# Optimization experiments

Hardware: AMD Instinct MI355X
Metric: run time of the kernel (lower is better)

Reference implementation:

```python
import jax, jax.numpy as jnp
import numpy as np

NUM_STEPS = 3
NUM_HEADS = 8
HEAD_DIM = 128
EPS = 1e-5


def layernorm(x, g, b):
    mu = jnp.mean(x, -1, keepdims=True)
    var = jnp.mean(jnp.square(x - mu), -1, keepdims=True)
    return (x - mu) * jax.lax.rsqrt(var + EPS) * g + b


def entmax15(x):
    # Exact entmax-1.5 along last axis (Peters & Martins 2019, sort-based).
    x = (x - jnp.max(x, -1, keepdims=True)) / 2.0
    xs = jnp.flip(jnp.sort(x, -1), -1)  # descending sort
    rho = jnp.arange(1, x.shape[-1] + 1, dtype=x.dtype)
    mean = jnp.cumsum(xs, -1) / rho
    meansq = jnp.cumsum(xs * xs, -1) / rho
    ss = rho * (meansq - jnp.square(mean))
    tau = mean - jnp.sqrt(jnp.clip((1.0 - ss) / rho, 0.0, None))
    support = jnp.sum(tau <= xs, -1, keepdims=True)
    tau_star = jnp.take_along_axis(tau, support - 1, -1)
    return jnp.square(jnp.clip(x - tau_star, 0.0, None))


def setup_inputs() -> dict:
    key = jax.random.key(0)
    ks = jax.random.split(key, 6)
    B, S, Hd, Md, N = 2, 1024, 2048, 1024, 2048
    THD = NUM_HEADS * HEAD_DIM
    return {
        "hidden": jax.random.normal(ks[0], (B, S, Hd), jnp.float32),
        "memory": jax.random.normal(ks[1], (N, Md), jnp.float32),
        "Wq": jax.random.normal(ks[2], (THD, Hd), jnp.float32) / np.float32(np.sqrt(Hd)),
        "Wk": jax.random.normal(ks[3], (THD, Md), jnp.float32) / np.float32(np.sqrt(Md)),
        "Wv": jax.random.normal(ks[4], (THD, Md), jnp.float32) / np.float32(np.sqrt(Md)),
        "Wo": jax.random.normal(ks[5], (Hd, THD), jnp.float32) / np.float32(np.sqrt(THD)),
        "log_beta": jnp.full((NUM_HEADS,), float(np.log(1.0 / np.sqrt(HEAD_DIM))), jnp.float32),
        "g_state": jnp.ones((Hd,), jnp.float32),
        "b_state": jnp.zeros((Hd,), jnp.float32),
        "g_mem": jnp.ones((Md,), jnp.float32),
        "b_mem": jnp.zeros((Md,), jnp.float32),
    }


def reference(hidden, memory, Wq, Wk, Wv, Wo, log_beta, g_state, b_state, g_mem, b_mem):
    B, S, _ = hidden.shape
    N = memory.shape[0]
    H, hd = NUM_HEADS, HEAD_DIM
    # projections
    Q = layernorm(hidden, g_state, b_state) @ Wq.T            # (B,S,H*hd)
    mn = layernorm(memory, g_mem, b_mem)                      # (N,Md)
    K = (mn @ Wk.T).reshape(N, H, hd).transpose(1, 0, 2)      # (H,N,hd)
    V = (mn @ Wv.T).reshape(N, H, hd).transpose(1, 0, 2)      # (H,N,hd)
    xi = Q.reshape(B, S, H, hd).transpose(0, 2, 1, 3)          # (B,H,S,hd)
    beta = jnp.exp(log_beta)[None, :, None, None]
    for _ in range(NUM_STEPS):
        scores = jnp.einsum('bhsd,hnd->bhsn', xi, K) * beta    # (B,H,S,N)
        w = entmax15(scores)
        xi = jnp.einsum('bhsn,hnd->bhsd', w, V)
    out = xi.transpose(0, 2, 1, 3).reshape(B, S, H * hd) @ Wo.T  # (B,S,hidden_dim)
    return out
```

## Files before the change

kernel.cpp:

```cpp
#include <hip/hip_runtime.h>

typedef _Float16 half8 __attribute__((ext_vector_type(8)));
typedef _Float16 hv4 __attribute__((ext_vector_type(4)));
typedef float fv4 __attribute__((ext_vector_type(4)));

typedef __attribute__((address_space(3))) unsigned lds_u32;
typedef const __attribute__((address_space(1))) unsigned glb_u32;

__device__ __forceinline__ void gll16(const void* g, void* l) {
  __builtin_amdgcn_global_load_lds((glb_u32*)g, (lds_u32*)l, 16, 0, 0);
}

__global__ __launch_bounds__(256) void ln_rows(const float* __restrict__ in,
                                               const float* __restrict__ g,
                                               const float* __restrict__ bb,
                                               _Float16* __restrict__ out, int ncols) {
  __shared__ float sm[8];
  int row = blockIdx.x, t = threadIdx.x;
  const float* rp = in + (size_t)row * ncols;
  int nv = ncols >> 10;
  fv4 v[2];
  float s1 = 0.f, s2 = 0.f;
#pragma unroll
  for (int c = 0; c < 2; ++c)
    if (c < nv) {
      v[c] = *(const fv4*)(rp + c * 1024 + t * 4);
#pragma unroll
      for (int j = 0; j < 4; ++j) { s1 += v[c][j]; s2 += v[c][j] * v[c][j]; }
    }
#pragma unroll
  for (int off = 32; off > 0; off >>= 1) { s1 += __shfl_xor(s1, off, 64); s2 += __shfl_xor(s2, off, 64); }
  int w = t >> 6;
  if ((t & 63) == 0) { sm[w] = s1; sm[4 + w] = s2; }
  __syncthreads();
  s1 = sm[0] + sm[1] + sm[2] + sm[3];
  s2 = sm[4] + sm[5] + sm[6] + sm[7];
  float inv = 1.0f / (float)ncols;
  float mu = s1 * inv;
  float var = s2 * inv - mu * mu;
  float rstd = rsqrtf(var + 1e-5f);
#pragma unroll
  for (int c = 0; c < 2; ++c)
    if (c < nv) {
      int col = c * 1024 + t * 4;
      fv4 gg = *(const fv4*)(g + col);
      fv4 bv = *(const fv4*)(bb + col);
      hv4 o;
#pragma unroll
      for (int j = 0; j < 4; ++j) o[j] = (_Float16)(((v[c][j] - mu) * rstd) * gg[j] + bv[j]);
      *(hv4*)(out + (size_t)row * ncols + col) = o;
    }
}

__global__ __launch_bounds__(256) void cast_f16(const float* __restrict__ in,
                                                _Float16* __restrict__ out, int n) {
  int i = (blockIdx.x * 256 + threadIdx.x) << 2;
  if (i < n) {
    fv4 f = *(const fv4*)(in + i);
    hv4 h;
#pragma unroll
    for (int j = 0; j < 4; ++j) h[j] = (_Float16)f[j];
    *(hv4*)(out + i) = h;
  }
}

__global__ __launch_bounds__(256) void reduce_split(const float* __restrict__ parts, int ns,
                                                    long long stride,
                                                    _Float16* __restrict__ hi, int n) {
  int i = (blockIdx.x * 256 + threadIdx.x) << 2;
  if (i < n) {
    fv4 s = *(const fv4*)(parts + i);
    for (int j = 1; j < ns; ++j) {
      fv4 v = *(const fv4*)(parts + (size_t)j * stride + i);
      s += v;
    }
    hv4 h;
#pragma unroll
    for (int j = 0; j < 4; ++j) h[j] = (_Float16)s[j];
    *(hv4*)(hi + i) = h;
  }
}

__global__ __launch_bounds__(256) void entmax_c(const _Float16* __restrict__ scores,
                                                float* __restrict__ crow) {
  __shared__ float comp[4][512];
  int wid = threadIdx.x >> 6;
  int row = blockIdx.x * 4 + wid;
  int l = threadIdx.x & 63;
  unsigned long long lmask = (1ull << l) - 1ull;
  const half8* sp = (const half8*)(scores + (size_t)row * 2048);
  half8 hx[4];
#pragma unroll
  for (int i = 0; i < 4; ++i) hx[i] = sp[i * 64 + l];
  fv4 x[8];
#pragma unroll
  for (int i = 0; i < 4; ++i)
#pragma unroll
    for (int j = 0; j < 8; ++j) x[i * 2 + (j >> 2)][j & 3] = (float)hx[i][j];
  float m = x[0][0];
#pragma unroll
  for (int i = 0; i < 8; ++i)
#pragma unroll
    for (int j = 0; j < 4; ++j) m = fmaxf(m, x[i][j]);
#pragma unroll
  for (int off = 32; off > 0; off >>= 1) m = fmaxf(m, __shfl_xor(m, off, 64));
#pragma unroll
  for (int i = 0; i < 8; ++i)
#pragma unroll
    for (int j = 0; j < 4; ++j) x[i][j] = (x[i][j] - m) * 0.5f;

  float tau = -1.0f;
  bool fixed = false;
  int cnti = 2048;
  for (int it = 0; it < 6 && !fixed; ++it) {
    float s1 = 0.f, s2 = 0.f;
    cnti = 0;
#pragma unroll
    for (int i = 0; i < 8; ++i)
#pragma unroll
      for (int j = 0; j < 4; ++j) {
        bool a = x[i][j] > tau;
        cnti += (int)__builtin_popcountll(__ballot(a));
        float sel = a ? x[i][j] : 0.f;
        s1 += sel;
        s2 = fmaf(sel, sel, s2);
      }
#pragma unroll
    for (int off = 32; off > 0; off >>= 1) {
      s1 += __shfl_xor(s1, off, 64);
      s2 += __shfl_xor(s2, off, 64);
    }
    float cnt = (float)cnti;
    float mean = s1 / cnt;
    float ss = s2 - s1 * mean;
    float nt = mean - sqrtf(fmaxf((1.0f - ss) / cnt, 0.0f));
    if (nt == tau) fixed = true;
    else tau = nt;
    if (cnti <= 512) break;
  }
  if (!fixed) {
    if (cnti <= 512) {
      int base = 0;
#pragma unroll
      for (int i = 0; i < 8; ++i)
#pragma unroll
        for (int j = 0; j < 4; ++j) {
          bool a = x[i][j] > tau;
          unsigned long long mk = __ballot(a);
          if (a) comp[wid][base + (int)__builtin_popcountll(mk & lmask)] = x[i][j];
          base += (int)__builtin_popcountll(mk);
        }
      float y[8];
#pragma unroll
      for (int r = 0; r < 8; ++r) {
        int idx = r * 64 + l;
        y[r] = (idx < base) ? comp[wid][idx] : -2.0f;
      }
      for (int it = 0; it < 10 && !fixed; ++it) {
        float s1 = 0.f, s2 = 0.f;
        int c = 0;
#pragma unroll
        for (int r = 0; r < 8; ++r) {
          bool a = y[r] > tau;
          c += (int)__builtin_popcountll(__ballot(a));
          float sel = a ? y[r] : 0.f;
          s1 += sel;
          s2 = fmaf(sel, sel, s2);
        }
#pragma unroll
        for (int off = 32; off > 0; off >>= 1) {
          s1 += __shfl_xor(s1, off, 64);
          s2 += __shfl_xor(s2, off, 64);
        }
        float cnt = (float)c;
        float mean = s1 / cnt;
        float ss = s2 - s1 * mean;
        float nt = mean - sqrtf(fmaxf((1.0f - ss) / cnt, 0.0f));
        if (nt == tau) fixed = true;
        else tau = nt;
      }
    } else {
      for (int it = 0; it < 8 && !fixed; ++it) {
        float s1 = 0.f, s2 = 0.f;
        int c = 0;
#pragma unroll
        for (int i = 0; i < 8; ++i)
#pragma unroll
          for (int j = 0; j < 4; ++j) {
            bool a = x[i][j] > tau;
            c += (int)__builtin_popcountll(__ballot(a));
            float sel = a ? x[i][j] : 0.f;
            s1 += sel;
            s2 = fmaf(sel, sel, s2);
          }
#pragma unroll
        for (int off = 32; off > 0; off >>= 1) {
          s1 += __shfl_xor(s1, off, 64);
          s2 += __shfl_xor(s2, off, 64);
        }
        float cnt = (float)c;
        float mean = s1 / cnt;
        float ss = s2 - s1 * mean;
        float nt = mean - sqrtf(fmaxf((1.0f - ss) / cnt, 0.0f));
        if (nt == tau) fixed = true;
        else tau = nt;
      }
    }
  }

  if (l == 0) crow[row] = 0.5f * m + tau;
}

struct GemmParams {
  const _Float16 *A, *B, *B2;
  const float* crow;
  _Float16 *C16, *C16b;
  float* C32;
  const float* log_beta;
  int K, lda, ldb;
  long long aSB, aSH, bSH;
  long long crowSB, crowSH;
  long long cSB, cSH, cOsR, cOsC;
  long long cOsRb, cOsCb;
  long long partStride;
  int alphaMode, outMode, outModeB, nsplit, dual;
};

template <int AMODE>
__global__ __launch_bounds__(256) void gemm_nt(GemmParams p) {
  constexpr int AST = AMODE ? 40 : 32;
  __shared__ __align__(16) _Float16 As[128 * AST];
  __shared__ __align__(16) _Float16 Bs[128 * 32];
  int t = threadIdx.x;
  int m0 = blockIdx.y * 128;
  int bx = blockIdx.x, n0, kbeg, kend, ks = 0;
  if (p.nsplit > 1) {
    ks = bx % p.nsplit;
    n0 = (bx / p.nsplit) * 128;
    int kl = p.K / p.nsplit;
    kbeg = ks * kl;
    kend = kbeg + kl;
  } else {
    n0 = bx * 128;
    kbeg = 0;
    kend = p.K;
  }
  int z = blockIdx.z, bidx, h, job = 0;
  if (p.dual) { job = z; bidx = 0; h = 0; }
  else { bidx = z >> 3; h = z & 7; }
  const _Float16* pA = p.A + bidx * p.aSB + h * p.aSH;
  const _Float16* pB = (job ? p.B2 : p.B) + h * p.bSH;
  const float* pc = AMODE ? p.crow + bidx * p.crowSB + h * p.crowSH : nullptr;

  fv4 acc[4][4] = {};
  int wv = t >> 6, l = t & 63, quad = l >> 4, lr = l & 15;
  int wm = (wv >> 1) * 64, wn = (wv & 1) * 64;
  int rl = l >> 2, cl = (l & 3) * 8;

  for (int k0 = kbeg; k0 < kend; k0 += 32) {
#pragma unroll
    for (int v = 0; v < 2; ++v) {
      int rb = wv * 16 + v * 64;
      int r = rb + rl;
      size_t aOff = (size_t)(m0 + r) * p.lda + k0 + cl;
      size_t bOff = (size_t)(n0 + r) * p.ldb + k0 + cl;
      if (AMODE == 0) {
        gll16(pA + aOff, &As[rb * 32]);
      } else {
        half8 s8 = *(const half8*)(pA + aOff);
        _Float16 c0 = (_Float16)pc[m0 + r];
        half8 d = s8 * (_Float16)0.5f - c0;
        d = __builtin_elementwise_max(d, (half8)(0));
        half8 w8 = d * d;
        *(half8*)&As[r * AST + cl] = w8;
      }
      gll16(pB + bOff, &Bs[rb * 32]);
    }
    __syncthreads();
    half8 ah[4], bh[4];
#pragma unroll
    for (int mi = 0; mi < 4; ++mi) ah[mi] = *(const half8*)&As[(wm + mi * 16 + lr) * AST + quad * 8];
#pragma unroll
    for (int ni = 0; ni < 4; ++ni) bh[ni] = *(const half8*)&Bs[(wn + ni * 16 + lr) * 32 + quad * 8];
#pragma unroll
    for (int mi = 0; mi < 4; ++mi)
#pragma unroll
      for (int ni = 0; ni < 4; ++ni)
        acc[mi][ni] = __builtin_amdgcn_mfma_f32_16x16x32_f16(ah[mi], bh[ni], acc[mi][ni], 0, 0, 0);
    __syncthreads();
  }

  float alpha = p.alphaMode ? __expf(p.log_beta[h]) : 1.0f;
  int om = (p.dual && job) ? p.outModeB : p.outMode;
  _Float16* c16 = (p.dual && job) ? p.C16b : p.C16;
  long long osR = (p.dual && job) ? p.cOsRb : p.cOsR;
  long long osC = (p.dual && job) ? p.cOsCb : p.cOsC;
  float* c32 = p.C32 + (p.nsplit > 1 ? (long long)ks * p.partStride : 0);
  long long cOff = (long long)bidx * p.cSB + (long long)h * p.cSH;
#pragma unroll
  for (int mi = 0; mi < 4; ++mi)
#pragma unroll
    for (int ni = 0; ni < 4; ++ni) {
      int row = m0 + wm + mi * 16 + quad * 4;
      int col = n0 + wn + ni * 16 + lr;
#pragma unroll
      for (int r = 0; r < 4; ++r) {
        float val = acc[mi][ni][r] * alpha;
        long long idx = cOff + (long long)(row + r) * osR + (long long)col * osC;
        if (om == 1) c32[idx] = val;
        else c16[idx] = (_Float16)val;
      }
    }
}

extern "C" void kernel_launch(void* const* d_in, const int* in_sizes, int n_in,
                              void* d_out, int out_size, void* d_ws, size_t ws_size,
                              hipStream_t stream) {
  const float* hidden = (const float*)d_in[0];
  const float* memory = (const float*)d_in[1];
  const float* Wq = (const float*)d_in[2];
  const float* Wk = (const float*)d_in[3];
  const float* Wv = (const float*)d_in[4];
  const float* Wo = (const float*)d_in[5];
  const float* log_beta = (const float*)d_in[6];
  const float* g_state = (const float*)d_in[7];
  const float* b_state = (const float*)d_in[8];
  const float* g_mem = (const float*)d_in[9];
  const float* b_mem = (const float*)d_in[10];

  char* w = (char*)d_ws;
  auto alloc = [&](size_t bytes) {
    char* r = w;
    w += (bytes + 255) & ~(size_t)255;
    return r;
  };
  _Float16* wq16 = (_Float16*)alloc(2097152 * 2);
  _Float16* wk16 = (_Float16*)alloc(1048576 * 2);
  _Float16* wv16 = (_Float16*)alloc(1048576 * 2);
  _Float16* wo16 = (_Float16*)alloc(2097152 * 2);
  _Float16* lnh16 = (_Float16*)alloc(4194304 * 2);
  _Float16* mn16 = (_Float16*)alloc(2097152 * 2);
  _Float16* kph = (_Float16*)alloc(2097152 * 2);
  _Float16* vt16 = (_Float16*)alloc(2097152 * 2);
  _Float16* xih = (_Float16*)alloc(2097152 * 2);
  float* parts = (float*)alloc((size_t)8 * 2097152 * 4);
  _Float16* scores16 = (_Float16*)alloc((size_t)33554432 * 2);
  float* crow = (float*)alloc(16384 * 4);

  ln_rows<<<2048, 256, 0, stream>>>(hidden, g_state, b_state, lnh16, 2048);
  ln_rows<<<2048, 256, 0, stream>>>(memory, g_mem, b_mem, mn16, 1024);
  cast_f16<<<2048, 256, 0, stream>>>(Wq, wq16, 2097152);
  cast_f16<<<1024, 256, 0, stream>>>(Wk, wk16, 1048576);
  cast_f16<<<1024, 256, 0, stream>>>(Wv, wv16, 1048576);
  cast_f16<<<2048, 256, 0, stream>>>(Wo, wo16, 2097152);

  {
    GemmParams p{};
    p.A = lnh16; p.lda = 2048;
    p.B = wq16; p.ldb = 2048;
    p.K = 2048; p.nsplit = 2;
    p.C32 = parts; p.outMode = 1; p.partStride = 2097152;
    p.cOsR = 1024; p.cOsC = 1;
    gemm_nt<0><<<dim3(16, 16, 1), 256, 0, stream>>>(p);
    reduce_split<<<2048, 256, 0, stream>>>(parts, 2, 2097152, xih, 2097152);
  }
  {
    GemmParams p{};
    p.A = mn16; p.lda = 1024;
    p.B = wk16; p.B2 = wv16; p.ldb = 1024;
    p.K = 1024; p.dual = 1;
    p.C16 = kph; p.outMode = 0; p.cOsR = 1024; p.cOsC = 1;
    p.C16b = vt16; p.outModeB = 0; p.cOsRb = 1; p.cOsCb = 2048;
    gemm_nt<0><<<dim3(8, 16, 2), 256, 0, stream>>>(p);
  }

  for (int step = 0; step < 3; ++step) {
    {
      GemmParams p{};
      p.A = xih;
      p.lda = 1024; p.aSB = 1048576; p.aSH = 128;
      p.B = kph; p.ldb = 1024; p.bSH = 128;
      p.K = 128;
      p.alphaMode = 1; p.log_beta = log_beta;
      p.C16 = scores16; p.outMode = 0;
      p.cSB = 16777216; p.cSH = 2097152;
      p.cOsR = 2048; p.cOsC = 1;
      gemm_nt<0><<<dim3(16, 8, 16), 256, 0, stream>>>(p);
    }
    entmax_c<<<4096, 256, 0, stream>>>(scores16, crow);
    {
      GemmParams p{};
      p.A = scores16; p.crow = crow;
      p.lda = 2048; p.aSB = 16777216; p.aSH = 2097152;
      p.crowSB = 8192; p.crowSH = 1024;
      p.B = vt16; p.ldb = 2048; p.bSH = 262144;
      p.K = 2048; p.nsplit = 4;
      p.C32 = parts; p.outMode = 1; p.partStride = 2097152;
      p.cSB = 1048576; p.cSH = 128;
      p.cOsR = 1024; p.cOsC = 1;
      gemm_nt<1><<<dim3(4, 8, 16), 256, 0, stream>>>(p);
    }
    reduce_split<<<2048, 256, 0, stream>>>(parts, 4, 2097152, xih, 2097152);
  }

  {
    GemmParams p{};
    p.A = xih; p.lda = 1024;
    p.B = wo16; p.ldb = 1024;
    p.K = 1024;
    p.C32 = (float*)d_out; p.outMode = 1;
    p.cOsR = 2048; p.cOsC = 1;
    gemm_nt<0><<<dim3(16, 16, 1), 256, 0, stream>>>(p);
  }
}
```

Before: 478.2 us.

## Double-buffer GEMM LDS, fuse prep launches, pair Q/KV GEMMs, swizzle blocks

Restructures the GEMM to double-buffer LDS tiles with async global-to-LDS loads and raises wave priority around the MFMA block. The entmax weight transform is moved from the global load path to the LDS read. Layernorm and weight cast kernels are merged into single launches, the Q and K/V projections run in one paired launch, and blocks are remapped so neighbouring tiles land on the same XCD. The aim is to hide load latency and cut launch overhead, at the cost of doubled LDS use and redundant transform arithmetic across waves.

```diff
diff --git a/kernel.cpp b/kernel.cpp
--- a/kernel.cpp
+++ b/kernel.cpp
@@ -11,12 +11,11 @@
   __builtin_amdgcn_global_load_lds((glb_u32*)g, (lds_u32*)l, 16, 0, 0);
 }
 
-__global__ __launch_bounds__(256) void ln_rows(const float* __restrict__ in,
-                                               const float* __restrict__ g,
-                                               const float* __restrict__ bb,
-                                               _Float16* __restrict__ out, int ncols) {
+__device__ __forceinline__ void ln_body(const float* __restrict__ in, const float* __restrict__ g,
+                                        const float* __restrict__ bb, _Float16* __restrict__ out,
+                                        int ncols, int row) {
   __shared__ float sm[8];
-  int row = blockIdx.x, t = threadIdx.x;
+  int t = threadIdx.x;
   const float* rp = in + (size_t)row * ncols;
   int nv = ncols >> 10;
   fv4 v[2];
@@ -52,16 +51,34 @@
     }
 }
 
-__global__ __launch_bounds__(256) void cast_f16(const float* __restrict__ in,
-                                                _Float16* __restrict__ out, int n) {
-  int i = (blockIdx.x * 256 + threadIdx.x) << 2;
-  if (i < n) {
-    fv4 f = *(const fv4*)(in + i);
-    hv4 h;
-#pragma unroll
-    for (int j = 0; j < 4; ++j) h[j] = (_Float16)f[j];
-    *(hv4*)(out + i) = h;
-  }
+__global__ __launch_bounds__(256) void ln_all(const float* __restrict__ hid,
+                                              const float* __restrict__ mem,
+                                              const float* __restrict__ gs, const float* __restrict__ bs,
+                                              const float* __restrict__ gm, const float* __restrict__ bm,
+                                              _Float16* __restrict__ oh, _Float16* __restrict__ om) {
+  int b = blockIdx.x;
+  if (b < 2048) ln_body(hid, gs, bs, oh, 2048, b);
+  else ln_body(mem, gm, bm, om, 1024, b - 2048);
+}
+
+__global__ __launch_bounds__(256) void cast_all(const float* __restrict__ s0, _Float16* __restrict__ d0,
+                                                const float* __restrict__ s1, _Float16* __restrict__ d1,
+                                                const float* __restrict__ s2, _Float16* __restrict__ d2,
+                                                const float* __restrict__ s3, _Float16* __restrict__ d3) {
+  int b = blockIdx.x;
+  const float* s;
+  _Float16* d;
+  int off;
+  if (b < 2048) { s = s0; d = d0; off = b; }
+  else if (b < 3072) { s = s1; d = d1; off = b - 2048; }
+  else if (b < 4096) { s = s2; d = d2; off = b - 3072; }
+  else { s = s3; d = d3; off = b - 4096; }
+  int i = (off * 256 + threadIdx.x) << 2;
+  fv4 f = *(const fv4*)(s + i);
+  hv4 h;
+#pragma unroll
+  for (int j = 0; j < 4; ++j) h[j] = (_Float16)f[j];
+  *(hv4*)(d + i) = h;
 }
 
 __global__ __launch_bounds__(256) void reduce_split(const float* __restrict__ parts, int ns,
@@ -224,16 +241,16 @@
   long long cOsRb, cOsCb;
   long long partStride;
   int alphaMode, outMode, outModeB, nsplit, dual;
+  int gx, gy, swz;
 };
 
 template <int AMODE>
-__global__ __launch_bounds__(256) void gemm_nt(GemmParams p) {
-  constexpr int AST = AMODE ? 40 : 32;
-  __shared__ __align__(16) _Float16 As[128 * AST];
-  __shared__ __align__(16) _Float16 Bs[128 * 32];
+__device__ __forceinline__ void gemm_body(const GemmParams& p, int bx, int by, int bz) {
+  __shared__ __align__(16) _Float16 As[2][128 * 32];
+  __shared__ __align__(16) _Float16 Bs[2][128 * 32];
   int t = threadIdx.x;
-  int m0 = blockIdx.y * 128;
-  int bx = blockIdx.x, n0, kbeg, kend, ks = 0;
+  int m0 = by * 128;
+  int n0, kbeg, kend, ks = 0;
   if (p.nsplit > 1) {
     ks = bx % p.nsplit;
     n0 = (bx / p.nsplit) * 128;
@@ -245,49 +262,63 @@
     kbeg = 0;
     kend = p.K;
   }
-  int z = blockIdx.z, bidx, h, job = 0;
-  if (p.dual) { job = z; bidx = 0; h = 0; }
-  else { bidx = z >> 3; h = z & 7; }
+  int bidx, h, job = 0;
+  if (p.dual) { job = bz; bidx = 0; h = 0; }
+  else { bidx = bz >> 3; h = bz & 7; }
   const _Float16* pA = p.A + bidx * p.aSB + h * p.aSH;
   const _Float16* pB = (job ? p.B2 : p.B) + h * p.bSH;
-  const float* pc = AMODE ? p.crow + bidx * p.crowSB + h * p.crowSH : nullptr;
 
   fv4 acc[4][4] = {};
   int wv = t >> 6, l = t & 63, quad = l >> 4, lr = l & 15;
   int wm = (wv >> 1) * 64, wn = (wv & 1) * 64;
   int rl = l >> 2, cl = (l & 3) * 8;
 
-  for (int k0 = kbeg; k0 < kend; k0 += 32) {
+  float cr[4];
+  if (AMODE == 1) {
+    const float* pc = p.crow + bidx * p.crowSB + h * p.crowSH;
+#pragma unroll
+    for (int mi = 0; mi < 4; ++mi) cr[mi] = pc[m0 + wm + mi * 16 + lr];
+  }
+
+  auto STAGE = [&](int buf, int k0) {
 #pragma unroll
     for (int v = 0; v < 2; ++v) {
       int rb = wv * 16 + v * 64;
       int r = rb + rl;
-      size_t aOff = (size_t)(m0 + r) * p.lda + k0 + cl;
-      size_t bOff = (size_t)(n0 + r) * p.ldb + k0 + cl;
-      if (AMODE == 0) {
-        gll16(pA + aOff, &As[rb * 32]);
-      } else {
-        half8 s8 = *(const half8*)(pA + aOff);
-        _Float16 c0 = (_Float16)pc[m0 + r];
-        half8 d = s8 * (_Float16)0.5f - c0;
+      gll16(pA + (size_t)(m0 + r) * p.lda + k0 + cl, &As[buf][rb * 32]);
+      gll16(pB + (size_t)(n0 + r) * p.ldb + k0 + cl, &Bs[buf][rb * 32]);
+    }
+  };
+
+  int nk = (kend - kbeg) >> 5;
+  STAGE(0, kbeg);
+  __syncthreads();
+  int cur = 0;
+  for (int ti = 0; ti < nk; ++ti) {
+    if (ti + 1 < nk) STAGE(cur ^ 1, kbeg + ((ti + 1) << 5));
+    half8 ah[4], bh[4];
+#pragma unroll
+    for (int mi = 0; mi < 4; ++mi) {
+      half8 a = *(const half8*)&As[cur][(wm + mi * 16 + lr) * 32 + quad * 8];
+      if (AMODE == 1) {
+        half8 d = a * (_Float16)0.5f - (_Float16)cr[mi];
         d = __builtin_elementwise_max(d, (half8)(0));
-        half8 w8 = d * d;
-        *(half8*)&As[r * AST + cl] = w8;
-      }
-      gll16(pB + bOff, &Bs[rb * 32]);
-    }
-    __syncthreads();
-    half8 ah[4], bh[4];
-#pragma unroll
-    for (int mi = 0; mi < 4; ++mi) ah[mi] = *(const half8*)&As[(wm + mi * 16 + lr) * AST + quad * 8];
-#pragma unroll
-    for (int ni = 0; ni < 4; ++ni) bh[ni] = *(const half8*)&Bs[(wn + ni * 16 + lr) * 32 + quad * 8];
+        a = d * d;
+      }
+      ah[mi] = a;
+    }
+#pragma unroll
+    for (int ni = 0; ni < 4; ++ni)
+      bh[ni] = *(const half8*)&Bs[cur][(wn + ni * 16 + lr) * 32 + quad * 8];
+    __builtin_amdgcn_s_setprio(1);
 #pragma unroll
     for (int mi = 0; mi < 4; ++mi)
 #pragma unroll
       for (int ni = 0; ni < 4; ++ni)
         acc[mi][ni] = __builtin_amdgcn_mfma_f32_16x16x32_f16(ah[mi], bh[ni], acc[mi][ni], 0, 0, 0);
+    __builtin_amdgcn_s_setprio(0);
     __syncthreads();
+    cur ^= 1;
   }
 
   float alpha = p.alphaMode ? __expf(p.log_beta[h]) : 1.0f;
@@ -311,6 +342,32 @@
         else c16[idx] = (_Float16)val;
       }
     }
+}
+
+template <int AMODE>
+__global__ __launch_bounds__(256) void gemm_nt(GemmParams p) {
+  int id = blockIdx.x;
+  if (p.swz) {
+    int q = (int)gridDim.x >> 3;
+    id = (id & 7) * q + (id >> 3);
+  }
+  int bx = id % p.gx;
+  int r = id / p.gx;
+  gemm_body<AMODE>(p, bx, r % p.gy, r / p.gy);
+}
+
+__global__ __launch_bounds__(256) void gemm_pair(GemmParams a, GemmParams b, int na) {
+  int id = blockIdx.x;
+  if (id < na) {
+    int bx = id % a.gx;
+    int r = id / a.gx;
+    gemm_body<0>(a, bx, r % a.gy, r / a.gy);
+  } else {
+    int j = id - na;
+    int bx = j % b.gx;
+    int r = j / b.gx;
+    gemm_body<0>(b, bx, r % b.gy, r / b.gy);
+  }
 }
 
 extern "C" void kernel_launch(void* const* d_in, const int* in_sizes, int n_in,
@@ -347,31 +404,28 @@
   _Float16* scores16 = (_Float16*)alloc((size_t)33554432 * 2);
   float* crow = (float*)alloc(16384 * 4);
 
-  ln_rows<<<2048, 256, 0, stream>>>(hidden, g_state, b_state, lnh16, 2048);
-  ln_rows<<<2048, 256, 0, stream>>>(memory, g_mem, b_mem, mn16, 1024);
-  cast_f16<<<2048, 256, 0, stream>>>(Wq, wq16, 2097152);
-  cast_f16<<<1024, 256, 0, stream>>>(Wk, wk16, 1048576);
-  cast_f16<<<1024, 256, 0, stream>>>(Wv, wv16, 1048576);
-  cast_f16<<<2048, 256, 0, stream>>>(Wo, wo16, 2097152);
+  ln_all<<<4096, 256, 0, stream>>>(hidden, memory, g_state, b_state, g_mem, b_mem, lnh16, mn16);
+  cast_all<<<6144, 256, 0, stream>>>(Wq, wq16, Wk, wk16, Wv, wv16, Wo, wo16);
 
   {
-    GemmParams p{};
-    p.A = lnh16; p.lda = 2048;
-    p.B = wq16; p.ldb = 2048;
-    p.K = 2048; p.nsplit = 2;
-    p.C32 = parts; p.outMode = 1; p.partStride = 2097152;
-    p.cOsR = 1024; p.cOsC = 1;
-    gemm_nt<0><<<dim3(16, 16, 1), 256, 0, stream>>>(p);
+    GemmParams pq{};
+    pq.A = lnh16; pq.lda = 2048;
+    pq.B = wq16; pq.ldb = 2048;
+    pq.K = 2048; pq.nsplit = 2;
+    pq.C32 = parts; pq.outMode = 1; pq.partStride = 2097152;
+    pq.cOsR = 1024; pq.cOsC = 1;
+    pq.gx = 16; pq.gy = 16;
+
+    GemmParams pkv{};
+    pkv.A = mn16; pkv.lda = 1024;
+    pkv.B = wk16; pkv.B2 = wv16; pkv.ldb = 1024;
+    pkv.K = 1024; pkv.dual = 1;
+    pkv.C16 = kph; pkv.outMode = 0; pkv.cOsR = 1024; pkv.cOsC = 1;
+    pkv.C16b = vt16; pkv.outModeB = 0; pkv.cOsRb = 1; pkv.cOsCb = 2048;
+    pkv.gx = 8; pkv.gy = 16;
+
+    gemm_pair<<<512, 256, 0, stream>>>(pq, pkv, 256);
     reduce_split<<<2048, 256, 0, stream>>>(parts, 2, 2097152, xih, 2097152);
-  }
-  {
-    GemmParams p{};
-    p.A = mn16; p.lda = 1024;
-    p.B = wk16; p.B2 = wv16; p.ldb = 1024;
-    p.K = 1024; p.dual = 1;
-    p.C16 = kph; p.outMode = 0; p.cOsR = 1024; p.cOsC = 1;
-    p.C16b = vt16; p.outModeB = 0; p.cOsRb = 1; p.cOsCb = 2048;
-    gemm_nt<0><<<dim3(8, 16, 2), 256, 0, stream>>>(p);
   }
 
   for (int step = 0; step < 3; ++step) {
@@ -385,7 +439,8 @@
       p.C16 = scores16; p.outMode = 0;
       p.cSB = 16777216; p.cSH = 2097152;
       p.cOsR = 2048; p.cOsC = 1;
-      gemm_nt<0><<<dim3(16, 8, 16), 256, 0, stream>>>(p);
+      p.gx = 16; p.gy = 8; p.swz = 1;
+      gemm_nt<0><<<2048, 256, 0, stream>>>(p);
     }
     entmax_c<<<4096, 256, 0, stream>>>(scores16, crow);
     {
@@ -398,7 +453,8 @@
       p.C32 = parts; p.outMode = 1; p.partStride = 2097152;
       p.cSB = 1048576; p.cSH = 128;
       p.cOsR = 1024; p.cOsC = 1;
-      gemm_nt<1><<<dim3(4, 8, 16), 256, 0, stream>>>(p);
+      p.gx = 4; p.gy = 8; p.swz = 1;
+      gemm_nt<1><<<512, 256, 0, stream>>>(p);
     }
     reduce_split<<<2048, 256, 0, stream>>>(parts, 4, 2097152, xih, 2097152);
   }
@@ -410,6 +466,7 @@
     p.K = 1024;
     p.C32 = (float*)d_out; p.outMode = 1;
     p.cOsR = 2048; p.cOsC = 1;
-    gemm_nt<0><<<dim3(16, 16, 1), 256, 0, stream>>>(p);
-  }
-}
+    p.gx = 16; p.gy = 16; p.swz = 1;
+    gemm_nt<0><<<256, 256, 0, stream>>>(p);
+  }
+}
```

Result: faster. 424.4 us (-11.2%).
